# Optimization experiments

Hardware: AMD Instinct MI355X
Metric: run time of the kernel (lower is better)

Reference implementation:

```python
import jax, jax.numpy as jnp
import numpy as np

NUM_HEADS = 32
NUM_KV_HEADS = 8
HEAD_DIM = 128
SEQ = 2048
MAX_SLOTS = 4096
SCALE = float(1.0 / np.sqrt(HEAD_DIM))  # attn_scale
G = NUM_HEADS // NUM_KV_HEADS  # num_queries_per_kv


def setup_inputs() -> dict:
    key = jax.random.key(0)
    k1, k2, k3 = jax.random.split(key, 3)
    q = jax.random.normal(k1, (SEQ, NUM_HEADS, HEAD_DIM), dtype=jnp.float32)
    k = jax.random.normal(k2, (SEQ, NUM_KV_HEADS, HEAD_DIM), dtype=jnp.float32)
    v = jax.random.normal(k3, (SEQ, NUM_KV_HEADS, HEAD_DIM), dtype=jnp.float32)
    k_cache = jnp.zeros((MAX_SLOTS, NUM_KV_HEADS, HEAD_DIM), dtype=jnp.float32)
    v_cache = jnp.zeros((MAX_SLOTS, NUM_KV_HEADS, HEAD_DIM), dtype=jnp.float32)
    slot_mapping = jnp.arange(SEQ, dtype=jnp.int64)  # contiguous block_table slots
    return {"q": q, "k": k, "v": v, "k_cache": k_cache, "v_cache": v_cache,
            "slot_mapping": slot_mapping}


def reference(q, k, v, k_cache, v_cache, slot_mapping):
    # prefill: scatter-write new K/V into the paged cache (self.k_cache[slot_mapping] = k)
    kc = k_cache.at[slot_mapping].set(k)
    vc = v_cache.at[slot_mapping].set(v)
    # gather K/V back from the cache via slot mapping (paged gather pattern)
    k_attn = kc[slot_mapping]  # (S, Hkv, D) == k since slots are unique
    v_attn = vc[slot_mapping]
    # GQA: repeat_interleave kv heads to match query heads
    kr = jnp.repeat(k_attn, G, axis=1)  # (S, H, D)
    vr = jnp.repeat(v_attn, G, axis=1)
    # scores: (H, Sq, Sk), naive full materialization as in the original
    scores = jnp.einsum('qhd,khd->hqk', q, kr) * SCALE
    sq, sk = q.shape[0], k_attn.shape[0]
    mask = jnp.tril(jnp.ones((sq, sk), dtype=bool))  # causal (num_query_tokens > 1)
    scores = jnp.where(mask[None, :, :], scores, -jnp.inf)
    weights = jax.nn.softmax(scores, axis=-1)
    out = jnp.einsum('hqk,khd->qhd', weights, vr)  # (S, H, D)
    return out
```

## Files before the change

### kernel.cpp

```cpp
#include <hip/hip_runtime.h>
#include <hip/hip_bf16.h>

#define SEQ 2048
#define QSTR 4096
#define CSCALE 0.1275174364688796f

typedef __attribute__((ext_vector_type(8)))  short short8;
typedef __attribute__((ext_vector_type(4)))  float f32x4;
typedef __attribute__((ext_vector_type(16))) float f32x16;

union PF8 { unsigned u[4]; short8 s; };

__device__ __forceinline__ unsigned short f2bf(float f) {
    union { __hip_bfloat16 b; unsigned short u; } cv;
    cv.b = __float2bfloat16(f);
    return cv.u;
}

__device__ __forceinline__ void gload16(const unsigned short* g, unsigned short* l) {
    __builtin_amdgcn_global_load_lds(
        (const __attribute__((address_space(1))) void*)g,
        (__attribute__((address_space(3))) void*)l, 16, 0, 0);
}

__global__ void prep_k(const float* __restrict__ Kg, unsigned short* __restrict__ Kb) {
    int gi = blockIdx.x * 256 + threadIdx.x;
    int kv = gi >> 8;
    int rem = gi & 255;
    int hk = rem >> 5;
    int d4 = rem & 31;
    f32x4 k4 = *(const f32x4*)(Kg + ((size_t)kv * 8 + hk) * 128 + 4 * d4);
    ushort4 u = make_ushort4(f2bf(k4[0]), f2bf(k4[1]), f2bf(k4[2]), f2bf(k4[3]));
    *(ushort4*)(Kb + ((size_t)hk * SEQ + kv) * 128 + 4 * d4) = u;
}

__global__ void prep_v(const float* __restrict__ Vg, unsigned short* __restrict__ Vtb) {
    const int hk  = blockIdx.x >> 5;
    const int kvb = blockIdx.x & 31;
    __shared__ unsigned short T[128][72];
    const int t = threadIdx.x;
    #pragma unroll
    for (int i = 0; i < 8; ++i) {
        int idx = t + 256 * i;
        int r = idx >> 5, d4 = idx & 31;
        f32x4 v = *(const f32x4*)(Vg + ((size_t)(kvb * 64 + r) * 8 + hk) * 128 + 4 * d4);
        T[4 * d4 + 0][r] = f2bf(v[0]);
        T[4 * d4 + 1][r] = f2bf(v[1]);
        T[4 * d4 + 2][r] = f2bf(v[2]);
        T[4 * d4 + 3][r] = f2bf(v[3]);
    }
    __syncthreads();
    #pragma unroll
    for (int i = 0; i < 8; ++i) {
        int idx = t + 256 * i;
        int d = idx >> 4, c4 = idx & 15;
        ushort4 u = *(ushort4*)&T[d][4 * c4];
        *(ushort4*)(Vtb + ((size_t)hk * 128 + d) * SEQ + kvb * 64 + 4 * c4) = u;
    }
}

__launch_bounds__(128, 2)
__global__ void attn_fwd(const float* __restrict__ Qg,
                         const unsigned short* __restrict__ Kb,
                         const unsigned short* __restrict__ Vtb,
                         float* __restrict__ Og) {
    const int bid = blockIdx.x;
    const int g   = bid >> 5;
    const int h   = bid & 31;
    const int hk  = h >> 2;
    int qb;
    if      (g < 8)  qb = 31 - g;
    else if (g < 16) qb = g - 8;
    else if (g < 24) qb = 39 - g;
    else             qb = g - 16;

    const int tid  = threadIdx.x;
    const int w    = tid >> 6;
    const int lane = tid & 63;
    const int q5   = lane & 31;
    const int t5   = lane >> 5;
    const int swz  = lane & 7;

    __shared__ __align__(16) unsigned char smem[32768];
    typedef unsigned short KsT[32][128];
    typedef unsigned short VtT[64][64];
    KsT* Ks = (KsT*)smem;
    VtT* Vt = (VtT*)(smem + 16384);
    float (*Ot)[132] = (float(*)[132])smem;

    const int q0w = qb * 64 + 32 * w;
    const int nt  = 2 * qb + 2;

    short8 qf[8];
    {
        const float* qp = Qg + (size_t)(q0w + q5) * QSTR + h * 128 + 8 * t5;
        #pragma unroll
        for (int st = 0; st < 8; ++st) {
            f32x4 a = *(const f32x4*)(qp + 16 * st);
            f32x4 b = *(const f32x4*)(qp + 16 * st + 4);
            short8 f;
            f[0] = (short)f2bf(a[0] * CSCALE); f[1] = (short)f2bf(a[1] * CSCALE);
            f[2] = (short)f2bf(a[2] * CSCALE); f[3] = (short)f2bf(a[3] * CSCALE);
            f[4] = (short)f2bf(b[0] * CSCALE); f[5] = (short)f2bf(b[1] * CSCALE);
            f[6] = (short)f2bf(b[2] * CSCALE); f[7] = (short)f2bf(b[3] * CSCALE);
            qf[st] = f;
        }
    }
    #pragma unroll
    for (int st = 0; st < 8; ++st) asm volatile("" :: "v"(qf[st]));
    asm volatile("s_waitcnt vmcnt(0)" ::: "memory");

    f32x16 oacc[4];
    #pragma unroll
    for (int dt = 0; dt < 4; ++dt)
        #pragma unroll
        for (int r = 0; r < 16; ++r) oacc[dt][r] = 0.f;
    float m = -1e30f, l = 0.f;

    auto ISSUE = [&](int t, int b) {
        const int kv0 = t * 32;
        #pragma unroll
        for (int p = 0; p < 4; ++p) {
            int row = 16 * w + 4 * p + (lane >> 4);
            const unsigned short* gp = Kb +
                ((size_t)hk * SEQ + kv0 + row) * 128 + 8 * ((lane & 15) ^ (row & 7));
            gload16(gp, &Ks[b][16 * w + 4 * p][0]);
        }
        #pragma unroll
        for (int p = 0; p < 4; ++p) {
            int d2 = 32 * w + 8 * p + (lane >> 3);
            int c  = (lane & 7) ^ (d2 & 7);
            int d  = d2 + 64 * (c >> 2);
            const unsigned short* gp = Vtb +
                ((size_t)hk * 128 + d) * SEQ + kv0 + 8 * (c & 3);
            gload16(gp, &Vt[b][32 * w + 8 * p][0]);
        }
    };

    ISSUE(0, 0);
    ISSUE(1, 1);

    for (int t = 0; t < nt; ++t) {
        const int kv0 = t * 32;
        const int buf = t & 1;
        if (t + 1 < nt) asm volatile("s_waitcnt vmcnt(8)" ::: "memory");
        else            asm volatile("s_waitcnt vmcnt(0)" ::: "memory");
        __builtin_amdgcn_s_barrier();

        const bool active = (kv0 <= q0w + 31);
        if (active) {
            f32x16 sac;
            #pragma unroll
            for (int r = 0; r < 16; ++r) sac[r] = 0.f;
            __builtin_amdgcn_s_setprio(1);
            #pragma unroll
            for (int st = 0; st < 8; ++st) {
                short8 kf = *(const short8*)&Ks[buf][q5][8 * ((2 * st + t5) ^ swz)];
                sac = __builtin_amdgcn_mfma_f32_32x32x16_bf16(kf, qf[st], sac, 0, 0, 0);
            }
            __builtin_amdgcn_s_setprio(0);

            if (kv0 + 31 > q0w) {
                const int qrow = q0w + q5;
                #pragma unroll
                for (int r = 0; r < 16; ++r) {
                    int kv = kv0 + (r & 3) + 8 * (r >> 2) + 4 * t5;
                    if (kv > qrow) sac[r] = -1e30f;
                }
            }

            float m8[8], m4[4], m2[2];
            #pragma unroll
            for (int i = 0; i < 8; ++i) m8[i] = fmaxf(sac[i], sac[i + 8]);
            #pragma unroll
            for (int i = 0; i < 4; ++i) m4[i] = fmaxf(m8[i], m8[i + 4]);
            m2[0] = fmaxf(m4[0], m4[2]); m2[1] = fmaxf(m4[1], m4[3]);
            float mx = fmaxf(m2[0], m2[1]);
            mx = fmaxf(mx, __shfl_xor(mx, 32));

            const bool skip = __all(mx <= m + 11.0f);
            float fac = 1.0f;
            if (!skip) {
                float mn = fmaxf(m, mx);
                fac = exp2f(m - mn);
                m = mn;
            }

            #pragma unroll
            for (int r = 0; r < 16; ++r) sac[r] = exp2f(sac[r] - m);
            float s8[8], s4[4], s2[2];
            #pragma unroll
            for (int i = 0; i < 8; ++i) s8[i] = sac[i] + sac[i + 8];
            #pragma unroll
            for (int i = 0; i < 4; ++i) s4[i] = s8[i] + s8[i + 4];
            s2[0] = s4[0] + s4[2]; s2[1] = s4[1] + s4[3];
            float ps = s2[0] + s2[1];
            ps += __shfl_xor(ps, 32);
            if (!skip) {
                l = l * fac + ps;
                #pragma unroll
                for (int dt = 0; dt < 4; ++dt)
                    #pragma unroll
                    for (int r = 0; r < 16; ++r) oacc[dt][r] *= fac;
            } else {
                l += ps;
            }

            unsigned pkw[8];
            #pragma unroll
            for (int rp = 0; rp < 8; ++rp)
                pkw[rp] = (unsigned)f2bf(sac[2 * rp]) |
                          ((unsigned)f2bf(sac[2 * rp + 1]) << 16);

            unsigned xp[8];
            #pragma unroll
            for (int i = 0; i < 8; ++i)
                xp[i] = (unsigned)__shfl_xor((int)pkw[i], 32);

            PF8 pf[2];
            #pragma unroll
            for (int ks = 0; ks < 2; ++ks) {
                #pragma unroll
                for (int j = 0; j < 4; ++j) {
                    const int ib = (j & 1) + 4 * ks;
                    const unsigned own_lo = pkw[ib];
                    const unsigned own_hi = pkw[ib + 2];
                    const unsigned par_lo = xp[ib];
                    const unsigned par_hi = xp[ib + 2];
                    pf[ks].u[j] = (j < 2) ? (t5 ? par_hi : own_lo)
                                          : (t5 ? own_hi : par_lo);
                }
            }

            __builtin_amdgcn_s_setprio(1);
            #pragma unroll
            for (int dt = 0; dt < 4; ++dt) {
                #pragma unroll
                for (int ks = 0; ks < 2; ++ks) {
                    short8 vf = *(const short8*)
                        &Vt[buf][32 * (dt & 1) + q5]
                           [8 * (((dt >> 1) * 4 + 2 * ks + t5) ^ swz)];
                    oacc[dt] = __builtin_amdgcn_mfma_f32_32x32x16_bf16(vf, pf[ks].s, oacc[dt], 0, 0, 0);
                }
            }
            __builtin_amdgcn_s_setprio(0);
        }

        asm volatile("" ::: "memory");
        __builtin_amdgcn_s_barrier();
        if (t + 2 < nt) ISSUE(t + 2, buf);
    }

    asm volatile("" ::: "memory");
    const float rl = 1.0f / l;
    #pragma unroll
    for (int pass = 0; pass < 2; ++pass) {
        if (w == pass) {
            #pragma unroll
            for (int dt = 0; dt < 4; ++dt)
                #pragma unroll
                for (int rq = 0; rq < 4; ++rq) {
                    f32x4 v;
                    v[0] = oacc[dt][4 * rq + 0] * rl;
                    v[1] = oacc[dt][4 * rq + 1] * rl;
                    v[2] = oacc[dt][4 * rq + 2] * rl;
                    v[3] = oacc[dt][4 * rq + 3] * rl;
                    *(f32x4*)&Ot[q5][32 * dt + 8 * rq + 4 * t5] = v;
                }
        }
        __syncthreads();
        {
            float* ob = Og + (size_t)(qb * 64 + pass * 32) * QSTR + h * 128;
            #pragma unroll
            for (int i = 0; i < 8; ++i) {
                int u = tid + 128 * i;
                int row = u >> 5, c4 = (u & 31) * 4;
                f32x4 v = *(const f32x4*)&Ot[row][c4];
                *(f32x4*)(ob + (size_t)row * QSTR + c4) = v;
            }
        }
        __syncthreads();
    }
}

extern "C" void kernel_launch(void* const* d_in, const int* in_sizes, int n_in,
                              void* d_out, int out_size, void* d_ws, size_t ws_size,
                              hipStream_t stream) {
    const float* q = (const float*)d_in[0];
    const float* k = (const float*)d_in[1];
    const float* v = (const float*)d_in[2];
    float* out = (float*)d_out;
    unsigned short* Kb  = (unsigned short*)d_ws;
    unsigned short* Vtb = Kb + (size_t)8 * SEQ * 128;
    prep_k<<<dim3(2048), 256, 0, stream>>>(k, Kb);
    prep_v<<<dim3(256), 256, 0, stream>>>(v, Vtb);
    attn_fwd<<<dim3(1024), 128, 0, stream>>>(q, Kb, Vtb, out);
}
```

Measured before the change: 101.7 us.

## Pair causal query blocks per workgroup and split KV tiles across four waves

Each workgroup now handles two complementary 64-row query blocks (p and 31-p), so every block runs a uniform 33 KV steps, which balances the causal triangle. It uses 256 threads, with two waves per query half each taking half of a 64-wide KV tile. The per-wave softmax partials are merged through shared-memory max/sum exchange in a new epilogue. The K and V LDS layouts and swizzles are reworked for 64-row tiles. The grid shrinks to 512 blocks and partial outputs are staged in bf16, which adds some rounding of the partial outputs and extra barriers.

Result: faster. 90.90 us (-10.6%).

```diff
diff --git a/kernel.cpp b/kernel.cpp
--- a/kernel.cpp
+++ b/kernel.cpp
@@ -15,6 +15,10 @@
     union { __hip_bfloat16 b; unsigned short u; } cv;
     cv.b = __float2bfloat16(f);
     return cv.u;
+}
+__device__ __forceinline__ float bf2f(unsigned short u) {
+    unsigned v = ((unsigned)u) << 16;
+    return __builtin_bit_cast(float, v);
 }
 
 __device__ __forceinline__ void gload16(const unsigned short* g, unsigned short* l) {
@@ -59,112 +63,193 @@
     }
 }
 
-__launch_bounds__(128, 2)
+__launch_bounds__(256, 2)
 __global__ void attn_fwd(const float* __restrict__ Qg,
                          const unsigned short* __restrict__ Kb,
                          const unsigned short* __restrict__ Vtb,
                          float* __restrict__ Og) {
     const int bid = blockIdx.x;
-    const int g   = bid >> 5;
+    const int p   = bid >> 5;
     const int h   = bid & 31;
     const int hk  = h >> 2;
-    int qb;
-    if      (g < 8)  qb = 31 - g;
-    else if (g < 16) qb = g - 8;
-    else if (g < 24) qb = 39 - g;
-    else             qb = g - 16;
+    const int qbB = 31 - p;
+    const int qbA = p;
+    const int nsB = 32 - p;
 
     const int tid  = threadIdx.x;
     const int w    = tid >> 6;
+    const int b    = w & 1;
+    const int hf   = w >> 1;
     const int lane = tid & 63;
     const int q5   = lane & 31;
     const int t5   = lane >> 5;
-    const int swz  = lane & 7;
-
-    __shared__ __align__(16) unsigned char smem[32768];
-    typedef unsigned short KsT[32][128];
-    typedef unsigned short VtT[64][64];
-    KsT* Ks = (KsT*)smem;
-    VtT* Vt = (VtT*)(smem + 16384);
-    float (*Ot)[132] = (float(*)[132])smem;
-
-    const int q0w = qb * 64 + 32 * w;
-    const int nt  = 2 * qb + 2;
+
+    __shared__ unsigned short Ks[2][64][128];
+    __shared__ unsigned short Vp[2][64][128];
+    __shared__ float mstat[2][4][32];
+    __shared__ unsigned short Otb[32][136];
 
     short8 qf[8];
-    {
-        const float* qp = Qg + (size_t)(q0w + q5) * QSTR + h * 128 + 8 * t5;
+    auto LOADQ = [&](int qb) __attribute__((always_inline)) {
+        const float* qp = Qg + (size_t)(qb * 64 + 32 * b + q5) * QSTR + h * 128 + 8 * t5;
         #pragma unroll
         for (int st = 0; st < 8; ++st) {
             f32x4 a = *(const f32x4*)(qp + 16 * st);
-            f32x4 b = *(const f32x4*)(qp + 16 * st + 4);
+            f32x4 c = *(const f32x4*)(qp + 16 * st + 4);
             short8 f;
             f[0] = (short)f2bf(a[0] * CSCALE); f[1] = (short)f2bf(a[1] * CSCALE);
             f[2] = (short)f2bf(a[2] * CSCALE); f[3] = (short)f2bf(a[3] * CSCALE);
-            f[4] = (short)f2bf(b[0] * CSCALE); f[5] = (short)f2bf(b[1] * CSCALE);
-            f[6] = (short)f2bf(b[2] * CSCALE); f[7] = (short)f2bf(b[3] * CSCALE);
+            f[4] = (short)f2bf(c[0] * CSCALE); f[5] = (short)f2bf(c[1] * CSCALE);
+            f[6] = (short)f2bf(c[2] * CSCALE); f[7] = (short)f2bf(c[3] * CSCALE);
             qf[st] = f;
         }
-    }
+    };
+
+    auto ISSUE = [&](int kv0, int bb) __attribute__((always_inline)) {
+        #pragma unroll
+        for (int p4 = 0; p4 < 4; ++p4) {
+            int row = 16 * w + 4 * p4 + (lane >> 4);
+            const unsigned short* g = Kb +
+                ((size_t)hk * SEQ + kv0 + row) * 128 + 8 * ((lane & 15) ^ (row & 15));
+            gload16(g, &Ks[bb][16 * w + 4 * p4][0]);
+        }
+        #pragma unroll
+        for (int p4 = 0; p4 < 4; ++p4) {
+            int r  = 16 * w + 4 * p4 + (lane >> 4);
+            int gg = lane & 15;
+            int d  = 2 * r + (gg >> 3);
+            int c  = (gg & 7) ^ (r & 7);
+            const unsigned short* g = Vtb +
+                ((size_t)hk * 128 + d) * SEQ + kv0 + 8 * c;
+            gload16(g, &Vp[bb][16 * w + 4 * p4][0]);
+        }
+    };
+
+    f32x16 oacc[4];
+    float m, l;
+    auto RESET = [&]() __attribute__((always_inline)) {
+        #pragma unroll
+        for (int dt = 0; dt < 4; ++dt)
+            #pragma unroll
+            for (int r = 0; r < 16; ++r) oacc[dt][r] = 0.f;
+        m = -1e30f; l = 0.f;
+    };
+
+    auto EPI = [&](int qb) __attribute__((always_inline)) {
+        if (t5 == 0) mstat[0][w][q5] = m;
+        asm volatile("s_waitcnt lgkmcnt(0)" ::: "memory");
+        __builtin_amdgcn_sched_barrier(0);
+        __builtin_amdgcn_s_barrier();
+        const float mo = mstat[0][w ^ 2][q5];
+        const float M  = fmaxf(m, mo);
+        const float sc = exp2f(m - M);
+        #pragma unroll
+        for (int dt = 0; dt < 4; ++dt)
+            #pragma unroll
+            for (int r = 0; r < 16; ++r) oacc[dt][r] *= sc;
+        const float lp = l * sc;
+        if (t5 == 0) mstat[1][w][q5] = lp;
+        asm volatile("s_waitcnt lgkmcnt(0)" ::: "memory");
+        __builtin_amdgcn_sched_barrier(0);
+        __builtin_amdgcn_s_barrier();
+        const float rl = 1.0f / (lp + mstat[1][w ^ 2][q5]);
+
+        #pragma unroll 1
+        for (int bb = 0; bb < 2; ++bb) {
+            if (w == 2 + bb) {
+                #pragma unroll
+                for (int dt = 0; dt < 4; ++dt)
+                    #pragma unroll
+                    for (int ii = 0; ii < 4; ++ii) {
+                        ushort4 u = make_ushort4(
+                            f2bf(oacc[dt][4 * ii + 0]), f2bf(oacc[dt][4 * ii + 1]),
+                            f2bf(oacc[dt][4 * ii + 2]), f2bf(oacc[dt][4 * ii + 3]));
+                        *(ushort4*)&Otb[q5][32 * dt + 8 * ii + 4 * t5] = u;
+                    }
+            }
+            asm volatile("s_waitcnt lgkmcnt(0)" ::: "memory");
+            __builtin_amdgcn_sched_barrier(0);
+            __builtin_amdgcn_s_barrier();
+            if (w == bb) {
+                #pragma unroll
+                for (int dt = 0; dt < 4; ++dt)
+                    #pragma unroll
+                    for (int ii = 0; ii < 4; ++ii) {
+                        ushort4 o1 = *(ushort4*)&Otb[q5][32 * dt + 8 * ii + 4 * t5];
+                        ushort4 u = make_ushort4(
+                            f2bf((oacc[dt][4 * ii + 0] + bf2f(o1.x)) * rl),
+                            f2bf((oacc[dt][4 * ii + 1] + bf2f(o1.y)) * rl),
+                            f2bf((oacc[dt][4 * ii + 2] + bf2f(o1.z)) * rl),
+                            f2bf((oacc[dt][4 * ii + 3] + bf2f(o1.w)) * rl));
+                        *(ushort4*)&Otb[q5][32 * dt + 8 * ii + 4 * t5] = u;
+                    }
+            }
+            asm volatile("s_waitcnt lgkmcnt(0)" ::: "memory");
+            __builtin_amdgcn_sched_barrier(0);
+            __builtin_amdgcn_s_barrier();
+            {
+                const int r  = tid >> 3;
+                const int c0 = 16 * (tid & 7);
+                float* og = Og + (size_t)(qb * 64 + 32 * bb + r) * QSTR + h * 128 + c0;
+                #pragma unroll
+                for (int j = 0; j < 4; ++j) {
+                    ushort4 u = *(ushort4*)&Otb[r][c0 + 4 * j];
+                    f32x4 v;
+                    v[0] = bf2f(u.x); v[1] = bf2f(u.y);
+                    v[2] = bf2f(u.z); v[3] = bf2f(u.w);
+                    *(f32x4*)(og + 4 * j) = v;
+                }
+            }
+            asm volatile("s_waitcnt lgkmcnt(0)" ::: "memory");
+            __builtin_amdgcn_sched_barrier(0);
+            __builtin_amdgcn_s_barrier();
+        }
+    };
+
+    LOADQ(qbB);
     #pragma unroll
     for (int st = 0; st < 8; ++st) asm volatile("" :: "v"(qf[st]));
     asm volatile("s_waitcnt vmcnt(0)" ::: "memory");
-
-    f32x16 oacc[4];
-    #pragma unroll
-    for (int dt = 0; dt < 4; ++dt)
-        #pragma unroll
-        for (int r = 0; r < 16; ++r) oacc[dt][r] = 0.f;
-    float m = -1e30f, l = 0.f;
-
-    auto ISSUE = [&](int t, int b) {
-        const int kv0 = t * 32;
-        #pragma unroll
-        for (int p = 0; p < 4; ++p) {
-            int row = 16 * w + 4 * p + (lane >> 4);
-            const unsigned short* gp = Kb +
-                ((size_t)hk * SEQ + kv0 + row) * 128 + 8 * ((lane & 15) ^ (row & 7));
-            gload16(gp, &Ks[b][16 * w + 4 * p][0]);
-        }
-        #pragma unroll
-        for (int p = 0; p < 4; ++p) {
-            int d2 = 32 * w + 8 * p + (lane >> 3);
-            int c  = (lane & 7) ^ (d2 & 7);
-            int d  = d2 + 64 * (c >> 2);
-            const unsigned short* gp = Vtb +
-                ((size_t)hk * 128 + d) * SEQ + kv0 + 8 * (c & 3);
-            gload16(gp, &Vt[b][32 * w + 8 * p][0]);
-        }
-    };
+    RESET();
 
     ISSUE(0, 0);
-    ISSUE(1, 1);
-
-    for (int t = 0; t < nt; ++t) {
-        const int kv0 = t * 32;
-        const int buf = t & 1;
-        if (t + 1 < nt) asm volatile("s_waitcnt vmcnt(8)" ::: "memory");
+    ISSUE(64, 1);
+
+    for (int s = 0; s < 33; ++s) {
+        if (s == nsB) {
+            LOADQ(qbA);
+            EPI(qbB);
+            RESET();
+        }
+        const bool isB = (s < nsB);
+        const int kv0  = isB ? 64 * s : 64 * (s - nsB);
+        const int qb   = isB ? qbB : qbA;
+        const int q0w  = qb * 64 + 32 * b;
+        const int buf  = s & 1;
+
+        if (s + 1 < 33) asm volatile("s_waitcnt vmcnt(8)" ::: "memory");
         else            asm volatile("s_waitcnt vmcnt(0)" ::: "memory");
         __builtin_amdgcn_s_barrier();
 
-        const bool active = (kv0 <= q0w + 31);
-        if (active) {
+        const int kvh = kv0 + 32 * hf;
+        if (kvh <= q0w + 31) {
             f32x16 sac;
             #pragma unroll
             for (int r = 0; r < 16; ++r) sac[r] = 0.f;
             __builtin_amdgcn_s_setprio(1);
             #pragma unroll
             for (int st = 0; st < 8; ++st) {
-                short8 kf = *(const short8*)&Ks[buf][q5][8 * ((2 * st + t5) ^ swz)];
+                short8 kf = *(const short8*)
+                    &Ks[buf][32 * hf + q5][8 * ((2 * st + t5) ^ (q5 & 15))];
                 sac = __builtin_amdgcn_mfma_f32_32x32x16_bf16(kf, qf[st], sac, 0, 0, 0);
             }
             __builtin_amdgcn_s_setprio(0);
 
-            if (kv0 + 31 > q0w) {
+            if (kvh + 31 > q0w) {
                 const int qrow = q0w + q5;
                 #pragma unroll
                 for (int r = 0; r < 16; ++r) {
-                    int kv = kv0 + (r & 3) + 8 * (r >> 2) + 4 * t5;
+                    int kv = kvh + (r & 3) + 8 * (r >> 2) + 4 * t5;
                     if (kv > qrow) sac[r] = -1e30f;
                 }
             }
@@ -237,9 +322,10 @@
             for (int dt = 0; dt < 4; ++dt) {
                 #pragma unroll
                 for (int ks = 0; ks < 2; ++ks) {
+                    const int gg = 8 * (q5 & 1) +
+                        ((4 * hf + 2 * ks + t5) ^ ((q5 >> 1) & 7));
                     short8 vf = *(const short8*)
-                        &Vt[buf][32 * (dt & 1) + q5]
-                           [8 * (((dt >> 1) * 4 + 2 * ks + t5) ^ swz)];
+                        &Vp[buf][16 * dt + (q5 >> 1)][8 * gg];
                     oacc[dt] = __builtin_amdgcn_mfma_f32_32x32x16_bf16(vf, pf[ks].s, oacc[dt], 0, 0, 0);
                 }
             }
@@ -248,39 +334,13 @@
 
         asm volatile("" ::: "memory");
         __builtin_amdgcn_s_barrier();
-        if (t + 2 < nt) ISSUE(t + 2, buf);
+        if (s + 2 < 33) {
+            const int s2 = s + 2;
+            ISSUE((s2 < nsB) ? 64 * s2 : 64 * (s2 - nsB), s & 1);
+        }
     }
 
-    asm volatile("" ::: "memory");
-    const float rl = 1.0f / l;
-    #pragma unroll
-    for (int pass = 0; pass < 2; ++pass) {
-        if (w == pass) {
-            #pragma unroll
-            for (int dt = 0; dt < 4; ++dt)
-                #pragma unroll
-                for (int rq = 0; rq < 4; ++rq) {
-                    f32x4 v;
-                    v[0] = oacc[dt][4 * rq + 0] * rl;
-                    v[1] = oacc[dt][4 * rq + 1] * rl;
-                    v[2] = oacc[dt][4 * rq + 2] * rl;
-                    v[3] = oacc[dt][4 * rq + 3] * rl;
-                    *(f32x4*)&Ot[q5][32 * dt + 8 * rq + 4 * t5] = v;
-                }
-        }
-        __syncthreads();
-        {
-            float* ob = Og + (size_t)(qb * 64 + pass * 32) * QSTR + h * 128;
-            #pragma unroll
-            for (int i = 0; i < 8; ++i) {
-                int u = tid + 128 * i;
-                int row = u >> 5, c4 = (u & 31) * 4;
-                f32x4 v = *(const f32x4*)&Ot[row][c4];
-                *(f32x4*)(ob + (size_t)row * QSTR + c4) = v;
-            }
-        }
-        __syncthreads();
-    }
+    EPI(qbA);
 }
 
 extern "C" void kernel_launch(void* const* d_in, const int* in_sizes, int n_in,
@@ -294,5 +354,5 @@
     unsigned short* Vtb = Kb + (size_t)8 * SEQ * 128;
     prep_k<<<dim3(2048), 256, 0, stream>>>(k, Kb);
     prep_v<<<dim3(256), 256, 0, stream>>>(v, Vtb);
-    attn_fwd<<<dim3(1024), 128, 0, stream>>>(q, Kb, Vtb, out);
-}
+    attn_fwd<<<dim3(512), 256, 0, stream>>>(q, Kb, Vtb, out);
+}
```
